# Kernel optimization log

Measured on AMD Instinct MI355X. Metric: run time of the kernel, lower is better.

The kernel has to match this reference:

```python
import jax, jax.numpy as jnp
import numpy as np

P_X = 2  # pooling window height
P_Y = 2  # pooling window width
SAMPLE_KEY = 42  # fixed key for the multinomial draw (torch uses global RNG)


def setup_inputs() -> dict:
    key = jax.random.key(0)
    k1, k2, k3 = jax.random.split(key, 3)
    P = P_X * P_Y
    c = jax.random.normal(k1, (16, 64, 256, 256), dtype=jnp.float32)
    # nn.Linear default init ~ U(-1/sqrt(fan_in), 1/sqrt(fan_in)); fan_in = P
    bound = 1.0 / np.sqrt(P)
    W1 = jax.random.uniform(k2, (P, P), jnp.float32, -bound, bound)
    W2 = jax.random.uniform(k3, (P, P), jnp.float32, -bound, bound)
    return {"c": c, "W1": W1, "W2": W2}


def reference(c, W1, W2):
    B, C, H, W = c.shape
    n, m = H // P_X, W // P_Y
    P = P_X * P_Y
    # [B,C,H,W] -> non-overlapping tiles [B,C,n,m,P], flattened row-major per tile
    tiles = c.reshape(B, C, n, P_X, m, P_Y).transpose(0, 1, 2, 4, 3, 5).reshape(B, C, n, m, P)
    # pooling_layer: Linear -> tanh -> Linear -> softmax (all over last dim, size P)
    h = jnp.tanh(jnp.einsum("bcnmp,qp->bcnmq", tiles, W1))
    logits = jnp.einsum("bcnmp,qp->bcnmq", h, W2)
    eta = jax.nn.softmax(logits, axis=-1)  # [B,C,n,m,P]
    # multinomial(eta, 1) == categorical sampling with logits (softmax-invariant)
    zeta = jax.random.categorical(jax.random.key(SAMPLE_KEY), logits, axis=-1)  # [B,C,n,m]
    pooled = jnp.take_along_axis(tiles, zeta[..., None], axis=-1)[..., 0]  # [B,C,n,m]
    return pooled, eta
```

## Files before the change

### kernel.cpp

```cpp
#include <hip/hip_runtime.h>
#include <math.h>


#define NTILES   16777216u
#define NBLOCKS  32768u

__device__ __forceinline__ unsigned rotl32(unsigned x, int r) {
  return (x << r) | (x >> (32 - r));
}

__device__ __forceinline__ unsigned tf_bits(unsigned i) {
  const unsigned k0 = 0u;
  const unsigned k1 = 42u;
  const unsigned k2 = 0x1BD11BDAu ^ 0u ^ 42u;
  unsigned x0 = 0u + k0;
  unsigned x1 = i + k1;
#define TF_ROUND(r) { x0 += x1; x1 = rotl32(x1, (r)); x1 ^= x0; }
  TF_ROUND(13) TF_ROUND(15) TF_ROUND(26) TF_ROUND(6)
  x0 += k1; x1 += k2 + 1u;
  TF_ROUND(17) TF_ROUND(29) TF_ROUND(16) TF_ROUND(24)
  x0 += k2; x1 += k0 + 2u;
  TF_ROUND(13) TF_ROUND(15) TF_ROUND(26) TF_ROUND(6)
  x0 += k0; x1 += k1 + 3u;
  TF_ROUND(17) TF_ROUND(29) TF_ROUND(16) TF_ROUND(24)
  x0 += k1; x1 += k2 + 4u;
  TF_ROUND(13) TF_ROUND(15) TF_ROUND(26) TF_ROUND(6)
  x0 += k2; x1 += k0 + 5u;
#undef TF_ROUND
  return x0 ^ x1;
}

__device__ __forceinline__ float xla_logf(float a) {
  unsigned b = __float_as_uint(a);
  int e = (int)(b >> 23) - 126;
  float m = __uint_as_float((b & 0x007fffffu) | 0x3f000000u);
  bool small = m < 0.70710678118654752440f;
  e -= small ? 1 : 0;
  float m1 = m - 1.0f;
  m = small ? (m1 + m) : m1;
  float z = m * m;
  float y = 7.0376836292e-2f;
  y = fmaf(y, m, -1.1514610310e-1f);
  y = fmaf(y, m,  1.1676998740e-1f);
  y = fmaf(y, m, -1.2420140846e-1f);
  y = fmaf(y, m,  1.4249322787e-1f);
  y = fmaf(y, m, -1.6668057665e-1f);
  y = fmaf(y, m,  2.0000714765e-1f);
  y = fmaf(y, m, -2.4999993993e-1f);
  y = fmaf(y, m,  3.3333331174e-1f);
  y = y * m;
  y = y * z;
  float ef = (float)e;
  y = fmaf(ef, -2.12194440e-4f, y);
  y = fmaf(-0.5f, z, y);
  float r = m + y;
  r = fmaf(ef, 0.693359375f, r);
  return r;
}

__device__ __forceinline__ float xla_tanhf(float x) {
  float ax = fabsf(x);
  float xc = fminf(fmaxf(x, -7.99881172180175781f), 7.99881172180175781f);
  float x2 = xc * xc;
  float num = -2.76076847742355e-16f;
  num = fmaf(x2, num,  2.00018790482477e-13f);
  num = fmaf(x2, num, -8.60467152213735e-11f);
  num = fmaf(x2, num,  5.12229709037114e-08f);
  num = fmaf(x2, num,  1.48572235717979e-05f);
  num = fmaf(x2, num,  6.37261928875436e-04f);
  num = fmaf(x2, num,  4.89352455891786e-03f);
  num = xc * num;
  float den = 1.19825839466702e-06f;
  den = fmaf(x2, den, 1.18534705686654e-04f);
  den = fmaf(x2, den, 2.26843463243900e-03f);
  den = fmaf(x2, den, 4.89352518554385e-03f);
  float r = num / den;
  return (ax < 0.0004f) ? x : r;
}

__device__ __forceinline__ float exact_gumbel(float u) {
  float tl = xla_logf(u);
  return -xla_logf(-tl);
}

__device__ __forceinline__ float fast_gumbel(float u) {
  float lg = __builtin_amdgcn_logf(u);
  float tn = lg * -0.69314718f;
  return __builtin_amdgcn_logf(tn) * -0.69314718f;
}

#define MARGIN_EPS 2.0e-4f

__device__ __forceinline__ void process_tile(
    unsigned t, float t0, float t1, float t2, float t3,
    const float* __restrict__ a1, const float* __restrict__ a2,
    float* __restrict__ pooled, float* __restrict__ eta) {
  float h[4];
#pragma unroll
  for (int q = 0; q < 4; ++q) {
    float acc = a1[q * 4 + 0] * t0;
    acc = fmaf(a1[q * 4 + 1], t1, acc);
    acc = fmaf(a1[q * 4 + 2], t2, acc);
    acc = fmaf(a1[q * 4 + 3], t3, acc);
    h[q] = xla_tanhf(acc);
  }
  float l[4];
#pragma unroll
  for (int q = 0; q < 4; ++q) {
    float acc = a2[q * 4 + 0] * h[0];
    acc = fmaf(a2[q * 4 + 1], h[1], acc);
    acc = fmaf(a2[q * 4 + 2], h[2], acc);
    acc = fmaf(a2[q * 4 + 3], h[3], acc);
    l[q] = acc;
  }

  float e0 = __builtin_amdgcn_exp2f(l[0] * 1.442695041f);
  float e1 = __builtin_amdgcn_exp2f(l[1] * 1.442695041f);
  float e2 = __builtin_amdgcn_exp2f(l[2] * 1.442695041f);
  float e3 = __builtin_amdgcn_exp2f(l[3] * 1.442695041f);
  float inv = __builtin_amdgcn_rcpf(((e0 + e1) + e2) + e3);

  unsigned base = 4u * t;
  float u[4];
#pragma unroll
  for (int q = 0; q < 4; ++q) {
    unsigned bits = tf_bits(base + (unsigned)q);
    float f = __uint_as_float((bits >> 9) | 0x3f800000u) - 1.0f;
    u[q] = (f == 0.0f) ? 1.17549435e-38f : f;
  }

  float best = fast_gumbel(u[0]) + l[0];
  float second = -3.402823466e+38f;
  int z = 0;
#pragma unroll
  for (int q = 1; q < 4; ++q) {
    float v = fast_gumbel(u[q]) + l[q];
    if (v > best) { second = best; best = v; z = q; }
    else if (v > second) { second = v; }
  }

  if (best - second < MARGIN_EPS) {
    float vb = exact_gumbel(u[0]) + l[0];
    z = 0;
#pragma unroll
    for (int q = 1; q < 4; ++q) {
      float v = exact_gumbel(u[q]) + l[q];
      if (v > vb) { vb = v; z = q; }
    }
  }

  float pv = t0;
  if (z == 1) pv = t1;
  if (z == 2) pv = t2;
  if (z == 3) pv = t3;

  pooled[t] = pv;
  *reinterpret_cast<float4*>(eta + (size_t)base) =
      make_float4(e0 * inv, e1 * inv, e2 * inv, e3 * inv);
}

__global__ __launch_bounds__(256) void pool_sample_kernel(
    const float* __restrict__ c,
    const float* __restrict__ w1,
    const float* __restrict__ w2,
    float* __restrict__ pooled,
    float* __restrict__ eta) {
  unsigned u = blockIdx.x * 256u + threadIdx.x;
  unsigned jj = u & 63u;
  unsigned i  = (u >> 6) & 127u;
  unsigned bc = u >> 13;

  float a1[16], a2[16];
#pragma unroll
  for (int k = 0; k < 16; ++k) { a1[k] = w1[k]; a2[k] = w2[k]; }

  size_t off = ((size_t)bc * 256u + 2u * i) * 256u + 4u * jj;
  float4 rA = *reinterpret_cast<const float4*>(c + off);
  float4 rB = *reinterpret_cast<const float4*>(c + off + 256u);

  unsigned t0 = (bc << 14) | (i << 7) | (jj << 1);
  process_tile(t0,     rA.x, rA.y, rB.x, rB.y, a1, a2, pooled, eta);
  process_tile(t0 + 1, rA.z, rA.w, rB.z, rB.w, a1, a2, pooled, eta);
}

extern "C" void kernel_launch(void* const* d_in, const int* in_sizes, int n_in,
                              void* d_out, int out_size, void* d_ws, size_t ws_size,
                              hipStream_t stream) {
  const float* c  = (const float*)d_in[0];
  const float* w1 = (const float*)d_in[1];
  const float* w2 = (const float*)d_in[2];
  float* pooled = (float*)d_out;
  float* eta    = (float*)d_out + (size_t)NTILES;

  pool_sample_kernel<<<dim3(NBLOCKS), dim3(256), 0, stream>>>(c, w1, w2, pooled, eta);
}
```

Before: 540.6 us.

## Pack two-tile MLP math into v2f FMAs with rcp-based tanh and exact fallback

Processes the two tiles per thread together using 2-wide float vectors so the compiler can emit packed FMA instructions for the two linear layers and the tanh polynomial. The tanh division is replaced with a hardware reciprocal times numerator. The exact path recomputes logits with the precise tanh only when the sampling margin is small. Pooled outputs are stored as a single float2. This reduces VALU instruction count but the approximate tanh feeds eta directly, which could shift softmax outputs slightly.

```diff
diff --git a/kernel.cpp b/kernel.cpp
--- a/kernel.cpp
+++ b/kernel.cpp
@@ -2,8 +2,14 @@
 #include <math.h>
 
 
-#define NTILES   16777216u
-#define NBLOCKS  32768u
+#define NTILES  16777216u
+#define NBLOCKS 32768u
+#define MARGIN_EPS 2.0e-4f
+
+typedef float v2f __attribute__((ext_vector_type(2)));
+
+__device__ __forceinline__ v2f s2(float v) { v2f r = {v, v}; return r; }
+#define PKFMA(a, b, c) __builtin_elementwise_fma((a), (b), (c))
 
 __device__ __forceinline__ unsigned rotl32(unsigned x, int r) {
   return (x << r) | (x >> (32 - r));
@@ -89,74 +95,81 @@
   return __builtin_amdgcn_logf(tn) * -0.69314718f;
 }
 
-#define MARGIN_EPS 2.0e-4f
-
-__device__ __forceinline__ void process_tile(
-    unsigned t, float t0, float t1, float t2, float t3,
-    const float* __restrict__ a1, const float* __restrict__ a2,
-    float* __restrict__ pooled, float* __restrict__ eta) {
-  float h[4];
-#pragma unroll
-  for (int q = 0; q < 4; ++q) {
-    float acc = a1[q * 4 + 0] * t0;
-    acc = fmaf(a1[q * 4 + 1], t1, acc);
-    acc = fmaf(a1[q * 4 + 2], t2, acc);
-    acc = fmaf(a1[q * 4 + 3], t3, acc);
-    h[q] = xla_tanhf(acc);
-  }
-  float l[4];
-#pragma unroll
-  for (int q = 0; q < 4; ++q) {
-    float acc = a2[q * 4 + 0] * h[0];
-    acc = fmaf(a2[q * 4 + 1], h[1], acc);
-    acc = fmaf(a2[q * 4 + 2], h[2], acc);
-    acc = fmaf(a2[q * 4 + 3], h[3], acc);
-    l[q] = acc;
-  }
-
-  float e0 = __builtin_amdgcn_exp2f(l[0] * 1.442695041f);
-  float e1 = __builtin_amdgcn_exp2f(l[1] * 1.442695041f);
-  float e2 = __builtin_amdgcn_exp2f(l[2] * 1.442695041f);
-  float e3 = __builtin_amdgcn_exp2f(l[3] * 1.442695041f);
-  float inv = __builtin_amdgcn_rcpf(((e0 + e1) + e2) + e3);
-
+__device__ __forceinline__ v2f pk_tanh_fast(v2f x) {
+  v2f xc = __builtin_elementwise_min(
+             __builtin_elementwise_max(x, s2(-7.99881172180175781f)),
+             s2(7.99881172180175781f));
+  v2f x2 = xc * xc;
+  v2f num = s2(-2.76076847742355e-16f);
+  num = PKFMA(x2, num, s2( 2.00018790482477e-13f));
+  num = PKFMA(x2, num, s2(-8.60467152213735e-11f));
+  num = PKFMA(x2, num, s2( 5.12229709037114e-08f));
+  num = PKFMA(x2, num, s2( 1.48572235717979e-05f));
+  num = PKFMA(x2, num, s2( 6.37261928875436e-04f));
+  num = PKFMA(x2, num, s2( 4.89352455891786e-03f));
+  num = xc * num;
+  v2f den = s2(1.19825839466702e-06f);
+  den = PKFMA(x2, den, s2(1.18534705686654e-04f));
+  den = PKFMA(x2, den, s2(2.26843463243900e-03f));
+  den = PKFMA(x2, den, s2(4.89352518554385e-03f));
+  float rx = num.x * __builtin_amdgcn_rcpf(den.x);
+  float ry = num.y * __builtin_amdgcn_rcpf(den.y);
+  v2f r;
+  r.x = (fabsf(x.x) < 0.0004f) ? x.x : rx;
+  r.y = (fabsf(x.y) < 0.0004f) ? x.y : ry;
+  return r;
+}
+
+__device__ __forceinline__ int sample_z(
+    unsigned t, float l0, float l1, float l2, float l3,
+    float s0, float s1, float s2v, float s3,
+    const float* __restrict__ a1, const float* __restrict__ a2) {
   unsigned base = 4u * t;
-  float u[4];
+  float uu[4];
 #pragma unroll
   for (int q = 0; q < 4; ++q) {
     unsigned bits = tf_bits(base + (unsigned)q);
     float f = __uint_as_float((bits >> 9) | 0x3f800000u) - 1.0f;
-    u[q] = (f == 0.0f) ? 1.17549435e-38f : f;
-  }
-
-  float best = fast_gumbel(u[0]) + l[0];
+    uu[q] = (f == 0.0f) ? 1.17549435e-38f : f;
+  }
+  float lf[4] = {l0, l1, l2, l3};
+  float best = fast_gumbel(uu[0]) + lf[0];
   float second = -3.402823466e+38f;
   int z = 0;
 #pragma unroll
   for (int q = 1; q < 4; ++q) {
-    float v = fast_gumbel(u[q]) + l[q];
+    float v = fast_gumbel(uu[q]) + lf[q];
     if (v > best) { second = best; best = v; z = q; }
     else if (v > second) { second = v; }
   }
-
   if (best - second < MARGIN_EPS) {
-    float vb = exact_gumbel(u[0]) + l[0];
+    float h[4];
+#pragma unroll
+    for (int q = 0; q < 4; ++q) {
+      float acc = a1[q * 4 + 0] * s0;
+      acc = fmaf(a1[q * 4 + 1], s1, acc);
+      acc = fmaf(a1[q * 4 + 2], s2v, acc);
+      acc = fmaf(a1[q * 4 + 3], s3, acc);
+      h[q] = xla_tanhf(acc);
+    }
+    float le[4];
+#pragma unroll
+    for (int q = 0; q < 4; ++q) {
+      float acc = a2[q * 4 + 0] * h[0];
+      acc = fmaf(a2[q * 4 + 1], h[1], acc);
+      acc = fmaf(a2[q * 4 + 2], h[2], acc);
+      acc = fmaf(a2[q * 4 + 3], h[3], acc);
+      le[q] = acc;
+    }
+    float vb = exact_gumbel(uu[0]) + le[0];
     z = 0;
 #pragma unroll
     for (int q = 1; q < 4; ++q) {
-      float v = exact_gumbel(u[q]) + l[q];
+      float v = exact_gumbel(uu[q]) + le[q];
       if (v > vb) { vb = v; z = q; }
     }
   }
-
-  float pv = t0;
-  if (z == 1) pv = t1;
-  if (z == 2) pv = t2;
-  if (z == 3) pv = t3;
-
-  pooled[t] = pv;
-  *reinterpret_cast<float4*>(eta + (size_t)base) =
-      make_float4(e0 * inv, e1 * inv, e2 * inv, e3 * inv);
+  return z;
 }
 
 __global__ __launch_bounds__(256) void pool_sample_kernel(
@@ -178,9 +191,65 @@
   float4 rA = *reinterpret_cast<const float4*>(c + off);
   float4 rB = *reinterpret_cast<const float4*>(c + off + 256u);
 
-  unsigned t0 = (bc << 14) | (i << 7) | (jj << 1);
-  process_tile(t0,     rA.x, rA.y, rB.x, rB.y, a1, a2, pooled, eta);
-  process_tile(t0 + 1, rA.z, rA.w, rB.z, rB.w, a1, a2, pooled, eta);
+  v2f t0 = {rA.x, rA.z};
+  v2f t1 = {rA.y, rA.w};
+  v2f t2 = {rB.x, rB.z};
+  v2f t3 = {rB.y, rB.w};
+
+  v2f h[4];
+#pragma unroll
+  for (int q = 0; q < 4; ++q) {
+    v2f acc = s2(a1[q * 4 + 0]) * t0;
+    acc = PKFMA(s2(a1[q * 4 + 1]), t1, acc);
+    acc = PKFMA(s2(a1[q * 4 + 2]), t2, acc);
+    acc = PKFMA(s2(a1[q * 4 + 3]), t3, acc);
+    h[q] = pk_tanh_fast(acc);
+  }
+  v2f l[4];
+#pragma unroll
+  for (int q = 0; q < 4; ++q) {
+    v2f acc = s2(a2[q * 4 + 0]) * h[0];
+    acc = PKFMA(s2(a2[q * 4 + 1]), h[1], acc);
+    acc = PKFMA(s2(a2[q * 4 + 2]), h[2], acc);
+    acc = PKFMA(s2(a2[q * 4 + 3]), h[3], acc);
+    l[q] = acc;
+  }
+
+  v2f e[4];
+#pragma unroll
+  for (int q = 0; q < 4; ++q) {
+    v2f ax = l[q] * s2(1.442695041f);
+    e[q].x = __builtin_amdgcn_exp2f(ax.x);
+    e[q].y = __builtin_amdgcn_exp2f(ax.y);
+  }
+  v2f sum = ((e[0] + e[1]) + e[2]) + e[3];
+  v2f inv;
+  inv.x = __builtin_amdgcn_rcpf(sum.x);
+  inv.y = __builtin_amdgcn_rcpf(sum.y);
+#pragma unroll
+  for (int q = 0; q < 4; ++q) e[q] = e[q] * inv;
+
+  unsigned tA = (bc << 14) | (i << 7) | (jj << 1);
+  int zA = sample_z(tA,     l[0].x, l[1].x, l[2].x, l[3].x,
+                    rA.x, rA.y, rB.x, rB.y, a1, a2);
+  int zB = sample_z(tA + 1, l[0].y, l[1].y, l[2].y, l[3].y,
+                    rA.z, rA.w, rB.z, rB.w, a1, a2);
+
+  float pvA = rA.x;
+  if (zA == 1) pvA = rA.y;
+  if (zA == 2) pvA = rB.x;
+  if (zA == 3) pvA = rB.y;
+  float pvB = rA.z;
+  if (zB == 1) pvB = rA.w;
+  if (zB == 2) pvB = rB.z;
+  if (zB == 3) pvB = rB.w;
+
+  *reinterpret_cast<float2*>(pooled + tA) = make_float2(pvA, pvB);
+  size_t ebase = 4u * (size_t)tA;
+  *reinterpret_cast<float4*>(eta + ebase) =
+      make_float4(e[0].x, e[1].x, e[2].x, e[3].x);
+  *reinterpret_cast<float4*>(eta + ebase + 4) =
+      make_float4(e[0].y, e[1].y, e[2].y, e[3].y);
 }
 
 extern "C" void kernel_launch(void* const* d_in, const int* in_sizes, int n_in,
```

New measurement: 542.2 us. Within noise of the previous version (+0.3%).
